# Performance work log

Measured on AMD Instinct MI355X. Metric: run time of the kernel, lower is better.

The kernel has to match this reference:

```python
import jax, jax.numpy as jnp
import numpy as np

IN_DIM, COND_DIM, OUT_DIM = 256, 256, 128
B, LQ, LK = 4, 4096, 4096


def setup_inputs() -> dict:
    key = jax.random.key(0)
    ks = jax.random.split(key, 8)
    s_in = 1.0 / np.sqrt(IN_DIM)
    s_c = 1.0 / np.sqrt(COND_DIM)
    return {
        "x": jax.random.normal(ks[0], (B, LQ, IN_DIM), dtype=jnp.float32),
        "cond": jax.random.normal(ks[1], (B, LK, COND_DIM), dtype=jnp.float32),
        "Wq": jax.random.uniform(ks[2], (IN_DIM, OUT_DIM), jnp.float32, -s_in, s_in),
        "bq": jax.random.uniform(ks[3], (OUT_DIM,), jnp.float32, -s_in, s_in),
        "Wk": jax.random.uniform(ks[4], (COND_DIM, OUT_DIM), jnp.float32, -s_c, s_c),
        "bk": jax.random.uniform(ks[5], (OUT_DIM,), jnp.float32, -s_c, s_c),
        "Wv": jax.random.uniform(ks[6], (COND_DIM, OUT_DIM), jnp.float32, -s_c, s_c),
        "bv": jax.random.uniform(ks[7], (OUT_DIM,), jnp.float32, -s_c, s_c),
    }


def reference(x, cond, Wq, bq, Wk, bk, Wv, bv):
    # q: [B, Lq, D], k/v: [B, Lk, D]
    q = jnp.einsum("bqi,id->bqd", x, Wq) + bq
    k = jnp.einsum("bkc,cd->bkd", cond, Wk) + bk
    v = jnp.einsum("bkc,cd->bkd", cond, Wv) + bv
    # NOTE: original uses UNscaled dot product (no 1/sqrt(d)).
    scores = jnp.einsum("bqd,bkd->bqk", q, k)  # [B, Lq, Lk]
    attn = jax.nn.softmax(scores, axis=-1)
    return jnp.einsum("bqk,bkd->bqd", attn, v)  # [B, Lq, D]
```

## Files before the change

kernel.cpp:

```cpp
#include <hip/hip_runtime.h>
#include <hip/hip_bf16.h>


typedef __attribute__((ext_vector_type(8))) short short8;
typedef __attribute__((ext_vector_type(8))) unsigned short ushort8;
typedef __attribute__((ext_vector_type(4))) unsigned short us4;
typedef __attribute__((ext_vector_type(4))) float f32x4;
typedef __attribute__((ext_vector_type(16))) float f32x16;
typedef __attribute__((ext_vector_type(4))) unsigned int u32x4;
typedef __bf16 bf16x8 __attribute__((ext_vector_type(8)));

constexpr int BATCH  = 4;
constexpr int SEQLEN = 4096;
constexpr int DIN    = 256;
constexpr int DOUT   = 128;
constexpr int ROWS   = BATCH * SEQLEN;
constexpr float LOG2E = 1.4426950408889634f;

static __device__ __forceinline__ unsigned short bf16_rn(float f) {
  unsigned int u = __builtin_bit_cast(unsigned int, f);
  unsigned int r = u + 0x7FFFu + ((u >> 16) & 1u);
  return (unsigned short)(r >> 16);
}
static __device__ __forceinline__ float bf16_f32(unsigned short h) {
  return __builtin_bit_cast(float, (unsigned int)h << 16);
}
static __device__ __forceinline__ float exp2n(float x) {
  return __builtin_amdgcn_exp2f(x);
}

static __device__ __forceinline__ f32x4 mfma_bf16(short8 a, short8 b, f32x4 c) {
  return __builtin_amdgcn_mfma_f32_16x16x32_bf16(
      __builtin_bit_cast(bf16x8, a), __builtin_bit_cast(bf16x8, b), c, 0, 0, 0);
}
static __device__ __forceinline__ f32x16 mfma32(short8 a, short8 b, f32x16 c) {
  return __builtin_amdgcn_mfma_f32_32x32x16_bf16(
      __builtin_bit_cast(bf16x8, a), __builtin_bit_cast(bf16x8, b), c, 0, 0, 0);
}

static __device__ __forceinline__ unsigned int cvt_pk(float lo, float hi) {
  unsigned int r;
  asm("v_cvt_pk_bf16_f32 %0, %1, %2" : "=v"(r) : "v"(lo), "v"(hi));
  return r;
}
static __device__ __forceinline__ void permswap(unsigned int& a, unsigned int& b) {
  asm("v_permlane32_swap_b32 %0, %1" : "+v"(a), "+v"(b));
}

static __device__ __forceinline__ int swz128(int a) {
  return a ^ (((a >> 7) & 7) << 4);
}
static __device__ __forceinline__ int swzK(int a) {
  return a ^ (((a >> 8) & 15) << 4);
}


__global__ __launch_bounds__(256) void proj_kernel(
    const float* __restrict__ x, const float* __restrict__ cond,
    const float* __restrict__ Wq, const float* __restrict__ bq,
    const float* __restrict__ Wk, const float* __restrict__ bk,
    const float* __restrict__ Wv, const float* __restrict__ bv,
    unsigned short* __restrict__ qb, unsigned short* __restrict__ kb,
    unsigned short* __restrict__ vt)
{
  const int which = blockIdx.y;
  const float* __restrict__ src  = (which == 0) ? x  : cond;
  const float* __restrict__ W    = (which == 0) ? Wq : (which == 1 ? Wk : Wv);
  const float* __restrict__ bias = (which == 0) ? bq : (which == 1 ? bk : bv);
  const int r0 = blockIdx.x * 64;

  __shared__ __align__(16) char lds[32768];
  char* const AhB = lds;
  char* const AlB = lds + 8192;
  char* const WtB = lds + 16384;

  const int tid  = threadIdx.x;
  const int wv   = tid >> 6;
  const int lane = tid & 63;
  const int g    = lane >> 4;
  const int c    = lane & 15;

  f32x4 acc[8];
  #pragma unroll
  for (int cf = 0; cf < 8; ++cf) acc[cf] = (f32x4){0.f, 0.f, 0.f, 0.f};

  for (int kt = 0; kt < 4; ++kt) {
    #pragma unroll
    for (int i = 0; i < 4; ++i) {
      const int idx = tid + i * 256;
      const int row = idx >> 4, f4 = idx & 15;
      const float4 a4 =
          *(const float4*)(src + (size_t)(r0 + row) * DIN + kt * 64 + f4 * 4);
      us4 hi, lo;
      const float av[4] = {a4.x, a4.y, a4.z, a4.w};
      #pragma unroll
      for (int e = 0; e < 4; ++e) {
        hi[e] = bf16_rn(av[e]);
        lo[e] = bf16_rn(av[e] - bf16_f32(hi[e]));
      }
      const int off = swz128(row * 128 + f4 * 8);
      *(us4*)(AhB + off) = hi;
      *(us4*)(AlB + off) = lo;
    }
    {
      const int col = tid & 127, half = tid >> 7;
      #pragma unroll
      for (int j = 0; j < 4; ++j) {
        const int k0 = half * 32 + j * 8;
        ushort8 wb;
        #pragma unroll
        for (int e = 0; e < 8; ++e)
          wb[e] = bf16_rn(W[(size_t)(kt * 64 + k0 + e) * DOUT + col]);
        *(ushort8*)(WtB + swz128(col * 128 + k0 * 2)) = wb;
      }
    }
    __syncthreads();

    #pragma unroll
    for (int ks = 0; ks < 2; ++ks) {
      const int aoff = (wv * 16 + c) * 128 + ks * 64 + g * 16;
      const short8 ah = *(const short8*)(AhB + swz128(aoff));
      const short8 al = *(const short8*)(AlB + swz128(aoff));
      #pragma unroll
      for (int cf = 0; cf < 8; ++cf) {
        const short8 wb =
            *(const short8*)(WtB + swz128((cf * 16 + c) * 128 + ks * 64 + g * 16));
        acc[cf] = mfma_bf16(ah, wb, acc[cf]);
        acc[cf] = mfma_bf16(al, wb, acc[cf]);
      }
    }
    __syncthreads();
  }

  if (which == 0) {
    #pragma unroll
    for (int cf = 0; cf < 8; ++cf) {
      const float bb = bias[cf * 16 + c];
      #pragma unroll
      for (int r = 0; r < 4; ++r)
        qb[(size_t)(r0 + wv * 16 + g * 4 + r) * DOUT + cf * 16 + c] =
            bf16_rn((acc[cf][r] + bb) * LOG2E);
    }
  } else if (which == 1) {
    char* const Ktile = lds;
    #pragma unroll
    for (int cf = 0; cf < 8; ++cf) {
      const float bb = bias[cf * 16 + c];
      #pragma unroll
      for (int r = 0; r < 4; ++r) {
        const int row = wv * 16 + g * 4 + r;
        *(unsigned short*)(Ktile + swzK(row * 256 + (cf * 16 + c) * 2)) =
            bf16_rn(acc[cf][r] + bb);
      }
    }
    __syncthreads();
    const int b2     = r0 >> 12;
    const int kblkG0 = (r0 & 4095) >> 5;
    #pragma unroll
    for (int j = 0; j < 4; ++j) {
      const int i    = tid + j * 256;
      const int kblk = i >> 9;
      const int rem  = i & 511;
      const int f    = rem >> 6;
      const int ln   = rem & 63;
      const int row  = kblk * 32 + (ln & 31);
      const int colb = f * 32 + (ln >> 5) * 16;
      const ushort8 v = *(const ushort8*)(Ktile + swzK(row * 256 + colb));
      *(ushort8*)((char*)kb +
          (((size_t)(b2 * 128 + kblkG0 + kblk) * 8 + f) * 64 + ln) * 16) = v;
    }
  } else {
    const int keybase = r0 + wv * 16 + g * 4;
    const int b2   = keybase >> 12;
    const int kblk = (keybase & 4095) >> 5;
    const int kk   = (keybase >> 4) & 1;
    const int h    = (keybase >> 3) & 1;
    const int e0   = keybase & 7;
    #pragma unroll
    for (int cf = 0; cf < 8; ++cf) {
      const float bb = bias[cf * 16 + c];
      const int col  = cf * 16 + c;
      const int dblk = col >> 5, l31 = col & 31;
      us4 pk;
      #pragma unroll
      for (int r = 0; r < 4; ++r) pk[r] = bf16_rn(acc[cf][r] + bb);
      *(us4*)(vt + (((((size_t)b2 * 128 + kblk) * 4 + dblk) * 2 + kk) * 64 +
                    h * 32 + l31) * 8 + e0) = pk;
    }
  }
}

constexpr int NSPLIT = 4;
constexpr int QBLK   = 32;
constexpr int KVBLK  = 32;
constexpr int ITERS  = SEQLEN / NSPLIT / KVBLK;

__global__ __launch_bounds__(256, 2) void attn_kernel(
    const unsigned short* __restrict__ qb,
    const unsigned short* __restrict__ kb,
    const unsigned short* __restrict__ vt,
    float* __restrict__ out)
{
  __shared__ __align__(16) float cmb[2][32][132];
  __shared__ float Ml[NSPLIT][32][2];

  const int bid = ((blockIdx.x & 7) << 6) | (blockIdx.x >> 3);
  const int qt  = bid & 127;
  const int b   = bid >> 7;
  const int tid = threadIdx.x;
  const int split = tid >> 6;
  const int lane  = tid & 63;
  const int ql = lane & 31;
  const int h  = lane >> 5;

  const int q0 = qt * QBLK;

  short8 qf[8];
  {
    const char* qp = (const char*)(qb + (size_t)(b * SEQLEN + q0 + ql) * DOUT) + h * 16;
    #pragma unroll
    for (int f = 0; f < 8; ++f) qf[f] = *(const short8*)(qp + f * 32);
  }

  const int kblk0 = split * (SEQLEN / NSPLIT / 32);
  const char* kfb = (const char*)kb + ((size_t)b * 128 + kblk0) * 8192 + lane * 16;
  const char* vfb = (const char*)vt + ((size_t)b * 128 + kblk0) * 8192 + lane * 16;

  f32x16 acc[4];
  #pragma unroll
  for (int d = 0; d < 4; ++d)
    #pragma unroll
    for (int r = 0; r < 16; ++r) acc[d][r] = 0.f;
  float mc = -1e30f, lc = 0.f;

  short8 kfA[8], kfB[8], vf[4][2];
  #pragma unroll
  for (int f = 0; f < 8; ++f) kfA[f] = *(const short8*)(kfb + f * 1024);
  #pragma unroll
  for (int f = 0; f < 8; ++f) kfB[f] = *(const short8*)(kfb + 8192 + f * 1024);
  kfb += 16384;
  #pragma unroll
  for (int d = 0; d < 4; ++d)
    #pragma unroll
    for (int kk = 0; kk < 2; ++kk)
      vf[d][kk] = *(const short8*)(vfb + (d * 2 + kk) * 1024);

  auto body = [&](short8 (&kf)[8], int t) {
    f32x16 s0, s1;
    #pragma unroll
    for (int r = 0; r < 16; ++r) { s0[r] = 0.f; s1[r] = 0.f; }
    __builtin_amdgcn_s_setprio(1);
    #pragma unroll
    for (int f = 0; f < 4; ++f) s0 = mfma32(kf[f], qf[f], s0);
    #pragma unroll
    for (int f = 0; f < 4; ++f) s1 = mfma32(kf[f + 4], qf[f + 4], s1);
    __builtin_amdgcn_s_setprio(0);

    if (t + 2 < ITERS) {
      #pragma unroll
      for (int f = 0; f < 8; ++f) kf[f] = *(const short8*)(kfb + f * 1024);
      kfb += 8192;
    }

    float s[16];
    #pragma unroll
    for (int r = 0; r < 16; ++r) s[r] = s0[r] + s1[r];

    float m01 = fmaxf(fmaxf(s[0],  s[1]),  s[2]);
    float m02 = fmaxf(fmaxf(s[3],  s[4]),  s[5]);
    float m03 = fmaxf(fmaxf(s[6],  s[7]),  s[8]);
    float m04 = fmaxf(fmaxf(s[9],  s[10]), s[11]);
    float m05 = fmaxf(fmaxf(s[12], s[13]), s[14]);
    float m11 = fmaxf(fmaxf(m01, m02), m03);
    float m12 = fmaxf(fmaxf(m04, m05), s[15]);
    float tm  = fmaxf(m11, m12);
    if (!__all(tm <= mc + 11.f)) {
      float tr = fmaxf(tm, __shfl_xor(tm, 32));
      const float mnew  = fmaxf(mc, tr);
      const float sc    = exp2n(mc - mnew);
      mc = mnew;
      lc *= sc;
      #pragma unroll
      for (int d = 0; d < 4; ++d)
        #pragma unroll
        for (int r = 0; r < 16; ++r) acc[d][r] *= sc;
    }
    float p[16];
    #pragma unroll
    for (int r = 0; r < 16; ++r) p[r] = exp2n(s[r] - mc);
    float a0 = (p[0]+p[1]) + (p[2]+p[3]);
    float a1 = (p[4]+p[5]) + (p[6]+p[7]);
    float a2 = (p[8]+p[9]) + (p[10]+p[11]);
    float a3 = (p[12]+p[13]) + (p[14]+p[15]);
    lc += (a0 + a1) + (a2 + a3);

    short8 pfrag[2];
    #pragma unroll
    for (int kk = 0; kk < 2; ++kk) {
      unsigned int A  = cvt_pk(p[kk * 8 + 0], p[kk * 8 + 1]);
      unsigned int Bv = cvt_pk(p[kk * 8 + 2], p[kk * 8 + 3]);
      unsigned int C  = cvt_pk(p[kk * 8 + 4], p[kk * 8 + 5]);
      unsigned int Dv = cvt_pk(p[kk * 8 + 6], p[kk * 8 + 7]);
      permswap(A, C);
      permswap(Bv, Dv);
      const u32x4 w = {A, Bv, C, Dv};
      pfrag[kk] = __builtin_bit_cast(short8, w);
    }

    __builtin_amdgcn_s_setprio(1);
    #pragma unroll
    for (int d = 0; d < 4; ++d)
      #pragma unroll
      for (int kk = 0; kk < 2; ++kk)
        acc[d] = mfma32(vf[d][kk], pfrag[kk], acc[d]);
    __builtin_amdgcn_s_setprio(0);

    if (t + 1 < ITERS) {
      vfb += 8192;
      #pragma unroll
      for (int d = 0; d < 4; ++d)
        #pragma unroll
        for (int kk = 0; kk < 2; ++kk)
          vf[d][kk] = *(const short8*)(vfb + (d * 2 + kk) * 1024);
    }
  };

  for (int t = 0; t < ITERS; t += 2) {
    body(kfA, t);
    body(kfB, t + 1);
  }

  lc += __shfl_xor(lc, 32);
  if (lane < 32) { Ml[split][ql][0] = mc; Ml[split][ql][1] = lc; }
  __syncthreads();

  float mg = -1e30f, lsum = 0.f;
  #pragma unroll
  for (int s2 = 0; s2 < NSPLIT; ++s2) mg = fmaxf(mg, Ml[s2][ql][0]);
  #pragma unroll
  for (int s2 = 0; s2 < NSPLIT; ++s2)
    lsum += Ml[s2][ql][1] * exp2n(Ml[s2][ql][0] - mg);
  const float fac = exp2n(mc - mg);
  #pragma unroll
  for (int d = 0; d < 4; ++d)
    #pragma unroll
    for (int r = 0; r < 16; ++r) acc[d][r] *= fac;

  if (split & 1) {
    float* reg = &cmb[split >> 1][0][0];
    #pragma unroll
    for (int d = 0; d < 4; ++d)
      #pragma unroll
      for (int rr = 0; rr < 4; ++rr) {
        const f32x4 v = {acc[d][rr*4+0], acc[d][rr*4+1], acc[d][rr*4+2], acc[d][rr*4+3]};
        *(f32x4*)(reg + ql * 132 + d * 32 + rr * 8 + h * 4) = v;
      }
  }
  __syncthreads();
  if (!(split & 1)) {
    const float* reg = &cmb[split >> 1][0][0];
    #pragma unroll
    for (int d = 0; d < 4; ++d)
      #pragma unroll
      for (int rr = 0; rr < 4; ++rr) {
        const f32x4 v = *(const f32x4*)(reg + ql * 132 + d * 32 + rr * 8 + h * 4);
        acc[d][rr*4+0] += v.x; acc[d][rr*4+1] += v.y;
        acc[d][rr*4+2] += v.z; acc[d][rr*4+3] += v.w;
      }
  }
  __syncthreads();
  if (split == 2) {
    float* reg = &cmb[0][0][0];
    #pragma unroll
    for (int d = 0; d < 4; ++d)
      #pragma unroll
      for (int rr = 0; rr < 4; ++rr) {
        const f32x4 v = {acc[d][rr*4+0], acc[d][rr*4+1], acc[d][rr*4+2], acc[d][rr*4+3]};
        *(f32x4*)(reg + ql * 132 + d * 32 + rr * 8 + h * 4) = v;
      }
  }
  __syncthreads();
  if (split == 0) {
    const float* reg = &cmb[0][0][0];
    const float inv = 1.f / lsum;
    float* const op = out + (size_t)(b * SEQLEN + q0 + ql) * DOUT;
    #pragma unroll
    for (int d = 0; d < 4; ++d)
      #pragma unroll
      for (int rr = 0; rr < 4; ++rr) {
        const f32x4 v = *(const f32x4*)(reg + ql * 132 + d * 32 + rr * 8 + h * 4);
        f32x4 o;
        o.x = (acc[d][rr*4+0] + v.x) * inv;
        o.y = (acc[d][rr*4+1] + v.y) * inv;
        o.z = (acc[d][rr*4+2] + v.z) * inv;
        o.w = (acc[d][rr*4+3] + v.w) * inv;
        *(f32x4*)(op + d * 32 + rr * 8 + h * 4) = o;
      }
  }
}

extern "C" void kernel_launch(void* const* d_in, const int* in_sizes, int n_in,
                              void* d_out, int out_size, void* d_ws, size_t ws_size,
                              hipStream_t stream) {
  const float* x    = (const float*)d_in[0];
  const float* cond = (const float*)d_in[1];
  const float* Wq   = (const float*)d_in[2];
  const float* bq   = (const float*)d_in[3];
  const float* Wk   = (const float*)d_in[4];
  const float* bk   = (const float*)d_in[5];
  const float* Wv   = (const float*)d_in[6];
  const float* bv   = (const float*)d_in[7];
  float* out = (float*)d_out;

  unsigned short* qb = (unsigned short*)d_ws;
  unsigned short* kb = qb + (size_t)ROWS * DOUT;
  unsigned short* vt = kb + (size_t)ROWS * DOUT;

  proj_kernel<<<dim3(ROWS / 64, 3), 256, 0, stream>>>(
      x, cond, Wq, bq, Wk, bk, Wv, bv, qb, kb, vt);

  attn_kernel<<<dim3(BATCH * (SEQLEN / QBLK)), 256, 0, stream>>>(
      qb, kb, vt, out);
}
```

Baseline: 71.42 us.

## Prepack projection weights once and software-pipeline QK^T one tile ahead

A small new kernel converts Wq/Wk/Wv to bf16 once, in MFMA fragment order, and writes them into the output buffer as scratch. The projection kernel then reads weight fragments directly from global memory instead of converting and staging them through LDS in every block, which removes redundant per-block weight conversion. The attention inner loop is restructured so the QK^T MFMAs for the next key tile are issued before the softmax of the current tile, to overlap matrix and vector work. The cost is an extra kernel launch, uncached-LDS global loads for weights, and more live registers for the second score accumulator.

```diff
diff --git a/kernel.cpp b/kernel.cpp
--- a/kernel.cpp
+++ b/kernel.cpp
@@ -55,24 +55,43 @@
 }
 
 
+__global__ __launch_bounds__(256) void wprep_kernel(
+    const float* __restrict__ Wq, const float* __restrict__ Wk,
+    const float* __restrict__ Wv, unsigned short* __restrict__ wtf)
+{
+  const float* __restrict__ W =
+      (blockIdx.x == 0) ? Wq : (blockIdx.x == 1 ? Wk : Wv);
+  unsigned short* const dst = wtf + (size_t)blockIdx.x * 32768;
+  #pragma unroll 4
+  for (int j = 0; j < 128; ++j) {
+    const int flat = j * 256 + threadIdx.x;
+    const int e    = flat & 7;
+    const int lane = (flat >> 3) & 63;
+    const int cf   = (flat >> 9) & 7;
+    const int ks   = (flat >> 12) & 1;
+    const int kt   = flat >> 13;
+    const int k    = kt * 64 + ks * 32 + (lane >> 4) * 8 + e;
+    const int col  = cf * 16 + (lane & 15);
+    dst[flat] = bf16_rn(W[(size_t)k * DOUT + col]);
+  }
+}
+
 __global__ __launch_bounds__(256) void proj_kernel(
     const float* __restrict__ x, const float* __restrict__ cond,
-    const float* __restrict__ Wq, const float* __restrict__ bq,
-    const float* __restrict__ Wk, const float* __restrict__ bk,
-    const float* __restrict__ Wv, const float* __restrict__ bv,
+    const float* __restrict__ bq, const float* __restrict__ bk,
+    const float* __restrict__ bv, const unsigned short* __restrict__ wtf,
     unsigned short* __restrict__ qb, unsigned short* __restrict__ kb,
     unsigned short* __restrict__ vt)
 {
   const int which = blockIdx.y;
   const float* __restrict__ src  = (which == 0) ? x  : cond;
-  const float* __restrict__ W    = (which == 0) ? Wq : (which == 1 ? Wk : Wv);
   const float* __restrict__ bias = (which == 0) ? bq : (which == 1 ? bk : bv);
+  const char* const wtfW = (const char*)wtf + which * 65536;
   const int r0 = blockIdx.x * 64;
 
   __shared__ __align__(16) char lds[32768];
   char* const AhB = lds;
   char* const AlB = lds + 8192;
-  char* const WtB = lds + 16384;
 
   const int tid  = threadIdx.x;
   const int wv   = tid >> 6;
@@ -102,18 +121,6 @@
       *(us4*)(AhB + off) = hi;
       *(us4*)(AlB + off) = lo;
     }
-    {
-      const int col = tid & 127, half = tid >> 7;
-      #pragma unroll
-      for (int j = 0; j < 4; ++j) {
-        const int k0 = half * 32 + j * 8;
-        ushort8 wb;
-        #pragma unroll
-        for (int e = 0; e < 8; ++e)
-          wb[e] = bf16_rn(W[(size_t)(kt * 64 + k0 + e) * DOUT + col]);
-        *(ushort8*)(WtB + swz128(col * 128 + k0 * 2)) = wb;
-      }
-    }
     __syncthreads();
 
     #pragma unroll
@@ -123,8 +130,8 @@
       const short8 al = *(const short8*)(AlB + swz128(aoff));
       #pragma unroll
       for (int cf = 0; cf < 8; ++cf) {
-        const short8 wb =
-            *(const short8*)(WtB + swz128((cf * 16 + c) * 128 + ks * 64 + g * 16));
+        const short8 wb = *(const short8*)(
+            wtfW + ((kt * 2 + ks) * 8 + cf) * 1024 + lane * 16);
         acc[cf] = mfma_bf16(ah, wb, acc[cf]);
         acc[cf] = mfma_bf16(al, wb, acc[cf]);
       }
@@ -245,39 +252,44 @@
     for (int kk = 0; kk < 2; ++kk)
       vf[d][kk] = *(const short8*)(vfb + (d * 2 + kk) * 1024);
 
-  auto body = [&](short8 (&kf)[8], int t) {
-    f32x16 s0, s1;
-    #pragma unroll
-    for (int r = 0; r < 16; ++r) { s0[r] = 0.f; s1[r] = 0.f; }
-    __builtin_amdgcn_s_setprio(1);
-    #pragma unroll
-    for (int f = 0; f < 4; ++f) s0 = mfma32(kf[f], qf[f], s0);
-    #pragma unroll
-    for (int f = 0; f < 4; ++f) s1 = mfma32(kf[f + 4], qf[f + 4], s1);
-    __builtin_amdgcn_s_setprio(0);
-
-    if (t + 2 < ITERS) {
-      #pragma unroll
-      for (int f = 0; f < 8; ++f) kf[f] = *(const short8*)(kfb + f * 1024);
+  f32x16 sA, sB;
+  #pragma unroll
+  for (int r = 0; r < 16; ++r) sA[r] = 0.f;
+  __builtin_amdgcn_s_setprio(1);
+  #pragma unroll
+  for (int f = 0; f < 8; ++f) sA = mfma32(kfA[f], qf[f], sA);
+  __builtin_amdgcn_s_setprio(0);
+  #pragma unroll
+  for (int f = 0; f < 8; ++f) kfA[f] = *(const short8*)(kfb + f * 1024);
+  kfb += 8192;
+
+  auto body = [&](f32x16& sCur, f32x16& sNext, short8 (&kfN)[8], int t) {
+    if (t + 1 < ITERS) {
+      #pragma unroll
+      for (int r = 0; r < 16; ++r) sNext[r] = 0.f;
+      __builtin_amdgcn_s_setprio(1);
+      #pragma unroll
+      for (int f = 0; f < 8; ++f) sNext = mfma32(kfN[f], qf[f], sNext);
+      __builtin_amdgcn_s_setprio(0);
+    }
+    if (t + 3 < ITERS) {
+      #pragma unroll
+      for (int f = 0; f < 8; ++f) kfN[f] = *(const short8*)(kfb + f * 1024);
       kfb += 8192;
     }
 
-    float s[16];
-    #pragma unroll
-    for (int r = 0; r < 16; ++r) s[r] = s0[r] + s1[r];
-
-    float m01 = fmaxf(fmaxf(s[0],  s[1]),  s[2]);
-    float m02 = fmaxf(fmaxf(s[3],  s[4]),  s[5]);
-    float m03 = fmaxf(fmaxf(s[6],  s[7]),  s[8]);
-    float m04 = fmaxf(fmaxf(s[9],  s[10]), s[11]);
-    float m05 = fmaxf(fmaxf(s[12], s[13]), s[14]);
+    float m01 = fmaxf(fmaxf(sCur[0],  sCur[1]),  sCur[2]);
+    float m02 = fmaxf(fmaxf(sCur[3],  sCur[4]),  sCur[5]);
+    float m03 = fmaxf(fmaxf(sCur[6],  sCur[7]),  sCur[8]);
+    float m04 = fmaxf(fmaxf(sCur[9],  sCur[10]), sCur[11]);
+    float m05 = fmaxf(fmaxf(sCur[12], sCur[13]), sCur[14]);
     float m11 = fmaxf(fmaxf(m01, m02), m03);
-    float m12 = fmaxf(fmaxf(m04, m05), s[15]);
+    float m12 = fmaxf(fmaxf(m04, m05), sCur[15]);
     float tm  = fmaxf(m11, m12);
     if (!__all(tm <= mc + 11.f)) {
       float tr = fmaxf(tm, __shfl_xor(tm, 32));
-      const float mnew  = fmaxf(mc, tr);
-      const float sc    = exp2n(mc - mnew);
+      const float mnew = fmaxf(mc, tr);
+      const float sc   = exp2n(mc - mnew);
       mc = mnew;
       lc *= sc;
       #pragma unroll
@@ -285,22 +297,21 @@
         #pragma unroll
         for (int r = 0; r < 16; ++r) acc[d][r] *= sc;
     }
-    float p[16];
-    #pragma unroll
-    for (int r = 0; r < 16; ++r) p[r] = exp2n(s[r] - mc);
-    float a0 = (p[0]+p[1]) + (p[2]+p[3]);
-    float a1 = (p[4]+p[5]) + (p[6]+p[7]);
-    float a2 = (p[8]+p[9]) + (p[10]+p[11]);
-    float a3 = (p[12]+p[13]) + (p[14]+p[15]);
+    #pragma unroll
+    for (int r = 0; r < 16; ++r) sCur[r] = exp2n(sCur[r] - mc);
+    float a0 = (sCur[0]+sCur[1]) + (sCur[2]+sCur[3]);
+    float a1 = (sCur[4]+sCur[5]) + (sCur[6]+sCur[7]);
+    float a2 = (sCur[8]+sCur[9]) + (sCur[10]+sCur[11]);
+    float a3 = (sCur[12]+sCur[13]) + (sCur[14]+sCur[15]);
     lc += (a0 + a1) + (a2 + a3);
 
     short8 pfrag[2];
     #pragma unroll
     for (int kk = 0; kk < 2; ++kk) {
-      unsigned int A  = cvt_pk(p[kk * 8 + 0], p[kk * 8 + 1]);
-      unsigned int Bv = cvt_pk(p[kk * 8 + 2], p[kk * 8 + 3]);
-      unsigned int C  = cvt_pk(p[kk * 8 + 4], p[kk * 8 + 5]);
-      unsigned int Dv = cvt_pk(p[kk * 8 + 6], p[kk * 8 + 7]);
+      unsigned int A  = cvt_pk(sCur[kk * 8 + 0], sCur[kk * 8 + 1]);
+      unsigned int Bv = cvt_pk(sCur[kk * 8 + 2], sCur[kk * 8 + 3]);
+      unsigned int C  = cvt_pk(sCur[kk * 8 + 4], sCur[kk * 8 + 5]);
+      unsigned int Dv = cvt_pk(sCur[kk * 8 + 6], sCur[kk * 8 + 7]);
       permswap(A, C);
       permswap(Bv, Dv);
       const u32x4 w = {A, Bv, C, Dv};
@@ -326,8 +337,8 @@
   };
 
   for (int t = 0; t < ITERS; t += 2) {
-    body(kfA, t);
-    body(kfB, t + 1);
+    body(sA, sB, kfB, t);
+    body(sB, sA, kfA, t + 1);
   }
 
   lc += __shfl_xor(lc, 32);
@@ -415,9 +426,12 @@
   unsigned short* qb = (unsigned short*)d_ws;
   unsigned short* kb = qb + (size_t)ROWS * DOUT;
   unsigned short* vt = kb + (size_t)ROWS * DOUT;
+  unsigned short* wtf = (unsigned short*)d_out;
+
+  wprep_kernel<<<dim3(3), 256, 0, stream>>>(Wq, Wk, Wv, wtf);
 
   proj_kernel<<<dim3(ROWS / 64, 3), 256, 0, stream>>>(
-      x, cond, Wq, bq, Wk, bk, Wv, bv, qb, kb, vt);
+      x, cond, bq, bk, bv, wtf, qb, kb, vt);
 
   attn_kernel<<<dim3(BATCH * (SEQLEN / QBLK)), 256, 0, stream>>>(
       qb, kb, vt, out);
```

New measurement: 90.26 us. 26.4% more time.

## Pre-convert weights into MFMA fragment layout in a prep kernel

Applied to the files above, without the earlier changes.

Adds a small kernel that converts Wq/Wk/Wv to bf16 once, in the exact per-lane MFMA fragment order, and stages them in the output buffer as scratch. The projection kernel then reads weight fragments straight from global memory instead of having every block gather, convert and stage them through LDS, which removes redundant strided loads and conversions per block. It also changes the attention kernel's occupancy hint to amdgpu_waves_per_eu(2,2). The trade-offs are one extra launch, and reuse of the output buffer as scratch, which relies on attn_kernel fully overwriting it later.

```diff
diff --git a/kernel.cpp b/kernel.cpp
--- a/kernel.cpp
+++ b/kernel.cpp
@@ -55,24 +55,45 @@
 }
 
 
+__global__ __launch_bounds__(256) void wprep_kernel(
+    const float* __restrict__ Wq, const float* __restrict__ Wk,
+    const float* __restrict__ Wv, unsigned short* __restrict__ wtf)
+{
+  const int which = blockIdx.x >> 5;
+  const int slice = blockIdx.x & 31;
+  const float* __restrict__ W =
+      (which == 0) ? Wq : (which == 1 ? Wk : Wv);
+  unsigned short* const dst = wtf + (size_t)which * 32768;
+  #pragma unroll
+  for (int j = 0; j < 4; ++j) {
+    const int flat = (slice * 4 + j) * 256 + threadIdx.x;
+    const int e    = flat & 7;
+    const int lane = (flat >> 3) & 63;
+    const int cf   = (flat >> 9) & 7;
+    const int ks   = (flat >> 12) & 1;
+    const int kt   = flat >> 13;
+    const int k    = kt * 64 + ks * 32 + (lane >> 4) * 8 + e;
+    const int col  = cf * 16 + (lane & 15);
+    dst[flat] = bf16_rn(W[(size_t)k * DOUT + col]);
+  }
+}
+
 __global__ __launch_bounds__(256) void proj_kernel(
     const float* __restrict__ x, const float* __restrict__ cond,
-    const float* __restrict__ Wq, const float* __restrict__ bq,
-    const float* __restrict__ Wk, const float* __restrict__ bk,
-    const float* __restrict__ Wv, const float* __restrict__ bv,
+    const float* __restrict__ bq, const float* __restrict__ bk,
+    const float* __restrict__ bv, const unsigned short* __restrict__ wtf,
     unsigned short* __restrict__ qb, unsigned short* __restrict__ kb,
     unsigned short* __restrict__ vt)
 {
   const int which = blockIdx.y;
   const float* __restrict__ src  = (which == 0) ? x  : cond;
-  const float* __restrict__ W    = (which == 0) ? Wq : (which == 1 ? Wk : Wv);
   const float* __restrict__ bias = (which == 0) ? bq : (which == 1 ? bk : bv);
+  const char* const wtfW = (const char*)wtf + which * 65536;
   const int r0 = blockIdx.x * 64;
 
   __shared__ __align__(16) char lds[32768];
   char* const AhB = lds;
   char* const AlB = lds + 8192;
-  char* const WtB = lds + 16384;
 
   const int tid  = threadIdx.x;
   const int wv   = tid >> 6;
@@ -102,18 +123,6 @@
       *(us4*)(AhB + off) = hi;
       *(us4*)(AlB + off) = lo;
     }
-    {
-      const int col = tid & 127, half = tid >> 7;
-      #pragma unroll
-      for (int j = 0; j < 4; ++j) {
-        const int k0 = half * 32 + j * 8;
-        ushort8 wb;
-        #pragma unroll
-        for (int e = 0; e < 8; ++e)
-          wb[e] = bf16_rn(W[(size_t)(kt * 64 + k0 + e) * DOUT + col]);
-        *(ushort8*)(WtB + swz128(col * 128 + k0 * 2)) = wb;
-      }
-    }
     __syncthreads();
 
     #pragma unroll
@@ -123,8 +132,8 @@
       const short8 al = *(const short8*)(AlB + swz128(aoff));
       #pragma unroll
       for (int cf = 0; cf < 8; ++cf) {
-        const short8 wb =
-            *(const short8*)(WtB + swz128((cf * 16 + c) * 128 + ks * 64 + g * 16));
+        const short8 wb = *(const short8*)(
+            wtfW + ((kt * 2 + ks) * 8 + cf) * 1024 + lane * 16);
         acc[cf] = mfma_bf16(ah, wb, acc[cf]);
         acc[cf] = mfma_bf16(al, wb, acc[cf]);
       }
@@ -195,7 +204,9 @@
 constexpr int KVBLK  = 32;
 constexpr int ITERS  = SEQLEN / NSPLIT / KVBLK;
 
-__global__ __launch_bounds__(256, 2) void attn_kernel(
+__global__ __launch_bounds__(256)
+__attribute__((amdgpu_waves_per_eu(2, 2)))
+void attn_kernel(
     const unsigned short* __restrict__ qb,
     const unsigned short* __restrict__ kb,
     const unsigned short* __restrict__ vt,
@@ -415,9 +426,12 @@
   unsigned short* qb = (unsigned short*)d_ws;
   unsigned short* kb = qb + (size_t)ROWS * DOUT;
   unsigned short* vt = kb + (size_t)ROWS * DOUT;
+  unsigned short* wtf = (unsigned short*)d_out;
+
+  wprep_kernel<<<dim3(96), 256, 0, stream>>>(Wq, Wk, Wv, wtf);
 
   proj_kernel<<<dim3(ROWS / 64, 3), 256, 0, stream>>>(
-      x, cond, Wq, bq, Wk, bk, Wv, bv, qb, kb, vt);
+      x, cond, bq, bk, bv, wtf, qb, kb, vt);
 
   attn_kernel<<<dim3(BATCH * (SEQLEN / QBLK)), 256, 0, stream>>>(
       qb, kb, vt, out);
```

Measured after the change: 84.36 us. +18.1%, slower.
